# Optimization experiments

Hardware: AMD Instinct MI355X
Metric: run time of the kernel (lower is better)

Reference implementation:

```python
import jax, jax.numpy as jnp
import numpy as np
import math

B, S, D = 1, 4096, 2048
H, KVH, HD = 32, 8, 64
W = 512            # sliding window size (== block size)
THETA = 10000.0
EPS = 1e-5
INTER = 5632
PRE_SCALE = 1.0 / math.sqrt(2.0)


def setup_inputs() -> dict:
    key = jax.random.key(0)
    ks = jax.random.split(key, 8)
    def w(k, shape, fan_in):
        return jax.random.normal(k, shape, jnp.float32) * (fan_in ** -0.5)
    return {
        "hidden_states": jax.random.normal(ks[0], (B, S, D), jnp.float32),
        "mixer_norm_w": jnp.ones((D,), jnp.float32),
        "wq": w(ks[1], (D, H * HD), D),
        "wk": w(ks[2], (D, KVH * HD), D),
        "wv": w(ks[3], (D, KVH * HD), D),
        "wo": w(ks[4], (H * HD, D), H * HD),
        "mlp_norm_w": jnp.ones((D,), jnp.float32),
        "w_gate": w(ks[5], (D, 2 * INTER), D),
        "w_down": w(ks[6], (INTER, D), INTER),
    }


def rmsnorm(x, w, eps=EPS):
    return x * jax.lax.rsqrt(jnp.mean(x * x, axis=-1, keepdims=True) + eps) * w


def rope(x):
    # x: [B, S, h, HD]; rotate-half RoPE
    half = HD // 2
    inv_freq = 1.0 / (THETA ** (jnp.arange(0, HD, 2, dtype=jnp.float32) / HD))
    freqs = jnp.arange(S, dtype=jnp.float32)[:, None] * inv_freq[None, :]  # [S, half]
    cos = jnp.cos(freqs)[None, :, None, :]
    sin = jnp.sin(freqs)[None, :, None, :]
    x1, x2 = x[..., :half], x[..., half:]
    return jnp.concatenate([x1 * cos - x2 * sin, x2 * cos + x1 * sin], axis=-1)


def sliding_attention(x, wq, wk, wv, wo):
    # x already pre-scaled; returns attn output (pre /pre_scale)
    q = (x @ wq).reshape(B, S, H, HD)
    k = (x @ wk).reshape(B, S, KVH, HD)
    v = (x @ wv).reshape(B, S, KVH, HD)
    q, k = rope(q), rope(k)
    rep = H // KVH
    k = jnp.repeat(k, rep, axis=2)  # [B,S,H,HD]
    v = jnp.repeat(v, rep, axis=2)
    nb = S // W
    qb = q.reshape(B, nb, W, H, HD)
    kb = k.reshape(B, nb, W, H, HD)
    vb = v.reshape(B, nb, W, H, HD)
    zeros = jnp.zeros((B, 1, W, H, HD), q.dtype)
    kw = jnp.concatenate([jnp.concatenate([zeros, kb[:, :-1]], axis=1), kb], axis=2)  # [B,nb,2W,H,HD]
    vw = jnp.concatenate([jnp.concatenate([zeros, vb[:, :-1]], axis=1), vb], axis=2)
    # local mask [nb, W, 2W]
    blk = jnp.arange(nb)[:, None, None]
    q_pos = blk * W + jnp.arange(W)[None, :, None]
    k_pos = blk * W - W + jnp.arange(2 * W)[None, None, :]
    mask = (k_pos >= 0) & (k_pos <= q_pos) & (q_pos - k_pos < W)
    scores = jnp.einsum("bnqhd,bnkhd->bhnqk", qb, kw) * (HD ** -0.5)
    scores = jnp.where(mask[None, None], scores, jnp.finfo(scores.dtype).min)
    p = jax.nn.softmax(scores, axis=-1)
    out = jnp.einsum("bhnqk,bnkhd->bnqhd", p, vw).reshape(B, S, H * HD)
    return out @ wo


def reference(hidden_states, mixer_norm_w, wq, wk, wv, wo, mlp_norm_w, w_gate, w_down):
    residual = hidden_states
    x = rmsnorm(hidden_states, mixer_norm_w)
    attn_out = sliding_attention(x * PRE_SCALE, wq, wk, wv, wo) / PRE_SCALE
    h = residual + attn_out
    xn = rmsnorm(h, mlp_norm_w)
    gv = xn @ w_gate
    gate, y = gv[..., :INTER], gv[..., INTER:]
    mlp_out = (jax.nn.silu(gate) * y) @ w_down
    return h + mlp_out
```

## Files before the change

### kernel.cpp

```cpp
#include <hip/hip_runtime.h>
#include <stdint.h>

typedef __attribute__((ext_vector_type(8))) short s16x8;
typedef __attribute__((ext_vector_type(4))) float f32x4;

#define GLD_LDS16(gp, lp) __builtin_amdgcn_global_load_lds( \
    (__attribute__((address_space(1))) void*)(void*)(gp), \
    (__attribute__((address_space(3))) void*)(lp), 16, 0, 0)

__device__ __forceinline__ float b2f(unsigned short s) {
    unsigned int u = ((unsigned int)s) << 16;
    return __builtin_bit_cast(float, u);
}
__device__ __forceinline__ unsigned short f2b(float f) {
    unsigned int u = __builtin_bit_cast(unsigned int, f);
    u = (u + 0x7FFFu + ((u >> 16) & 1u)) >> 16;
    return (unsigned short)u;
}
__device__ __forceinline__ f32x4 mfma16(s16x8 a, s16x8 b, f32x4 c) {
    return __builtin_amdgcn_mfma_f32_16x16x32_bf16(a, b, c, 0, 0, 0);
}

__global__ __launch_bounds__(256) void rmsnorm_bf16(
    const float* __restrict__ x, const float* __restrict__ wgt,
    unsigned short* __restrict__ out)
{
    const int row = blockIdx.x;
    const int t = threadIdx.x;
    const float* xr = x + (size_t)row * 2048;
    float4 a = *(const float4*)(xr + t * 8);
    float4 b = *(const float4*)(xr + t * 8 + 4);
    float ss = a.x*a.x + a.y*a.y + a.z*a.z + a.w*a.w
             + b.x*b.x + b.y*b.y + b.z*b.z + b.w*b.w;
    #pragma unroll
    for (int d = 1; d < 64; d <<= 1) ss += __shfl_xor(ss, d);
    __shared__ float red[4];
    if ((t & 63) == 0) red[t >> 6] = ss;
    __syncthreads();
    float tot = red[0] + red[1] + red[2] + red[3];
    float inv = rsqrtf(tot * (1.0f / 2048.0f) + 1e-5f);
    float vals[8] = {a.x, a.y, a.z, a.w, b.x, b.y, b.z, b.w};
    const float* wr_ = wgt + t * 8;
    s16x8 ov;
    #pragma unroll
    for (int j = 0; j < 8; ++j) ov[j] = (short)f2b(vals[j] * inv * wr_[j]);
    *(s16x8*)(out + (size_t)row * 2048 + t * 8) = ov;
}

__global__ __launch_bounds__(256) void transpose_to_bf16(
    const float* __restrict__ in, unsigned short* __restrict__ out, int K, int N)
{
    __shared__ float tile[64][65];
    const int n0 = blockIdx.x * 64, k0 = blockIdx.y * 64;
    const int t = threadIdx.x;
    const int kr = t >> 4, nc = (t & 15) * 4;
    #pragma unroll
    for (int i = 0; i < 4; ++i) {
        float4 v = *(const float4*)(in + (size_t)(k0 + kr + i * 16) * N + n0 + nc);
        tile[nc + 0][kr + i * 16] = v.x;
        tile[nc + 1][kr + i * 16] = v.y;
        tile[nc + 2][kr + i * 16] = v.z;
        tile[nc + 3][kr + i * 16] = v.w;
    }
    __syncthreads();
    const int nr = t >> 3, kc = (t & 7) * 8;
    #pragma unroll
    for (int p = 0; p < 2; ++p) {
        s16x8 o;
        #pragma unroll
        for (int j = 0; j < 8; ++j) o[j] = (short)f2b(tile[nr + p * 32][kc + j]);
        *(s16x8*)(out + (size_t)(n0 + nr + p * 32) * K + k0 + kc) = o;
    }
}

template <int BN, int EPI>
__global__ __launch_bounds__(512, 2) void gemmq(
    const unsigned short* __restrict__ A,
    const unsigned short* __restrict__ B,
    void* __restrict__ Cv,
    const float* __restrict__ ADD,
    const float2* __restrict__ RT,
    int N, int K)
{
    constexpr int WN  = BN / 4;
    constexpr int HN  = WN / 2;
    constexpr int NJQ = WN / 32;
    constexpr int NBU = BN / 64;
    constexpr int ABUF = 256 * 64;
    constexpr int BBUF = BN * 64;
    __shared__ __align__(16) unsigned short As[2 * ABUF];
    __shared__ __align__(16) unsigned short Bs[2 * BBUF];

    const int t = threadIdx.x;
    const int l = t & 63, w = t >> 6;
    const int l15 = l & 15, lg = l >> 4;
    const int wr = w >> 2, wc = w & 3;
    const int x7 = l15 & 7;
    const int cc0 = ((lg) ^ x7) << 3;
    const int cc1 = ((4 | lg) ^ x7) << 3;

    const int nwg = (int)gridDim.x;
    const int orig = (int)blockIdx.x;
    const int q8 = nwg >> 3, r8 = nwg & 7;
    const int xcd = orig & 7, lid = orig >> 3;
    const int wg = (xcd < r8 ? xcd * (q8 + 1) : r8 * (q8 + 1) + (xcd - r8) * q8) + lid;
    const int m0 = (wg & 15) * 256;
    const int n0 = (wg >> 4) * BN;

    const int tr = t >> 3;
    const int scol = ((t & 7) ^ (tr & 7)) << 3;
    const unsigned short* pA[4];
    #pragma unroll
    for (int u = 0; u < 4; ++u) {
        const int lrow = u * 64 + tr;
        const int g = ((lrow >> 6) & 1) * 128 + (lrow >> 7) * 64 + (lrow & 63);
        pA[u] = A + (size_t)(m0 + g) * K + scol;
    }
    const unsigned short* pB[NBU];
    #pragma unroll
    for (int u = 0; u < NBU; ++u) {
        const int lrow = u * 64 + tr;
        const int h = lrow / (BN / 2), rem = lrow % (BN / 2);
        const int g = (rem / HN) * WN + h * HN + (rem % HN);
        pB[u] = B + (size_t)(n0 + g) * K + scol;
    }

    f32x4 acc[2][2][4][NJQ] = {};
    s16x8 aF[4][2];
    s16x8 bF[2][NJQ][2];

    const int NT = K / 64;

    #pragma unroll
    for (int u = 0; u < 4; ++u) GLD_LDS16(pA[u], &As[u * 4096 + t * 8]);
    #pragma unroll
    for (int u = 0; u < NBU; ++u) GLD_LDS16(pB[u], &Bs[u * 4096 + t * 8]);
    asm volatile("s_waitcnt vmcnt(0)" ::: "memory");
    __builtin_amdgcn_s_barrier();

    for (int kt = 0; kt < NT; ++kt) {
        const int rb  = (kt & 1) ? ABUF : 0;
        const int rbB = (kt & 1) ? BBUF : 0;
        const int wb  = ABUF - rb;
        const int wbB = BBUF - rbB;
        const int knext = (kt + 1 < NT ? kt + 1 : kt) * 64;

        #pragma unroll
        for (int i = 0; i < 4; ++i) {
            const int lr = wr * 64 + i * 16 + l15;
            aF[i][0] = *(const s16x8*)&As[rb + lr * 64 + cc0];
            aF[i][1] = *(const s16x8*)&As[rb + lr * 64 + cc1];
        }
        #pragma unroll
        for (int j = 0; j < NJQ; ++j) {
            const int lr = wc * HN + j * 16 + l15;
            bF[0][j][0] = *(const s16x8*)&Bs[rbB + lr * 64 + cc0];
            bF[0][j][1] = *(const s16x8*)&Bs[rbB + lr * 64 + cc1];
        }
        #pragma unroll
        for (int u = 0; u < 4; ++u)
            GLD_LDS16(pA[u] + knext, &As[wb + u * 4096 + t * 8]);
        #pragma unroll
        for (int kk = 0; kk < 2; ++kk)
            #pragma unroll
            for (int i = 0; i < 4; ++i)
                #pragma unroll
                for (int j = 0; j < NJQ; ++j)
                    acc[0][0][i][j] = mfma16(aF[i][kk], bF[0][j][kk], acc[0][0][i][j]);

        #pragma unroll
        for (int j = 0; j < NJQ; ++j) {
            const int lr = (BN / 2) + wc * HN + j * 16 + l15;
            bF[1][j][0] = *(const s16x8*)&Bs[rbB + lr * 64 + cc0];
            bF[1][j][1] = *(const s16x8*)&Bs[rbB + lr * 64 + cc1];
        }
        #pragma unroll
        for (int u = 0; u < NBU; ++u)
            GLD_LDS16(pB[u] + knext, &Bs[wbB + u * 4096 + t * 8]);
        #pragma unroll
        for (int kk = 0; kk < 2; ++kk)
            #pragma unroll
            for (int i = 0; i < 4; ++i)
                #pragma unroll
                for (int j = 0; j < NJQ; ++j)
                    acc[0][1][i][j] = mfma16(aF[i][kk], bF[1][j][kk], acc[0][1][i][j]);

        #pragma unroll
        for (int i = 0; i < 4; ++i) {
            const int lr = 128 + wr * 64 + i * 16 + l15;
            aF[i][0] = *(const s16x8*)&As[rb + lr * 64 + cc0];
            aF[i][1] = *(const s16x8*)&As[rb + lr * 64 + cc1];
        }
        #pragma unroll
        for (int kk = 0; kk < 2; ++kk)
            #pragma unroll
            for (int i = 0; i < 4; ++i)
                #pragma unroll
                for (int j = 0; j < NJQ; ++j)
                    acc[1][0][i][j] = mfma16(aF[i][kk], bF[0][j][kk], acc[1][0][i][j]);

        #pragma unroll
        for (int kk = 0; kk < 2; ++kk)
            #pragma unroll
            for (int i = 0; i < 4; ++i)
                #pragma unroll
                for (int j = 0; j < NJQ; ++j)
                    acc[1][1][i][j] = mfma16(aF[i][kk], bF[1][j][kk], acc[1][1][i][j]);

        asm volatile("s_waitcnt vmcnt(0)" ::: "memory");
        __builtin_amdgcn_s_barrier();
    }

    if constexpr (EPI == 2) {
        unsigned short* Cb = (unsigned short*)Cv;
        const bool roped = (n0 < 2560);
        #pragma unroll
        for (int qm = 0; qm < 2; ++qm)
            #pragma unroll
            for (int i = 0; i < 4; ++i)
                #pragma unroll
                for (int r = 0; r < 4; ++r) {
                    const int row = m0 + wr * 128 + qm * 64 + i * 16 + lg * 4 + r;
                    const size_t rbase = (size_t)row * N;
                    #pragma unroll
                    for (int j = 0; j < NJQ; ++j) {
                        const int d = j * 16 + l15;
                        const int c0 = n0 + wc * WN + j * 16 + l15;
                        float a = acc[qm][0][i][j][r];
                        float b = acc[qm][1][i][j][r];
                        if (roped) {
                            float2 cs = RT[row * 32 + d];
                            Cb[rbase + c0]      = f2b(a * cs.x - b * cs.y);
                            Cb[rbase + c0 + HN] = f2b(b * cs.x + a * cs.y);
                        } else {
                            Cb[rbase + c0]      = f2b(a);
                            Cb[rbase + c0 + HN] = f2b(b);
                        }
                    }
                }
    } else {
        #pragma unroll
        for (int qm = 0; qm < 2; ++qm)
            #pragma unroll
            for (int i = 0; i < 4; ++i)
                #pragma unroll
                for (int r = 0; r < 4; ++r) {
                    const int row = m0 + wr * 128 + qm * 64 + i * 16 + lg * 4 + r;
                    const size_t rbase = (size_t)row * N;
                    #pragma unroll
                    for (int qn = 0; qn < 2; ++qn)
                        #pragma unroll
                        for (int j = 0; j < NJQ; ++j) {
                            const int col = n0 + wc * WN + qn * HN + j * 16 + l15;
                            float v = acc[qm][qn][i][j][r];
                            if constexpr (EPI == 0) {
                                ((unsigned short*)Cv)[rbase + col] = f2b(v);
                            } else {
                                ((float*)Cv)[rbase + col] = v + ADD[rbase + col];
                            }
                        }
                }
    }
}

__global__ __launch_bounds__(512, 2) void gemm_glu(
    const unsigned short* __restrict__ A,
    const unsigned short* __restrict__ Bg,
    const unsigned short* __restrict__ By,
    unsigned short* __restrict__ act,
    int N, int K)
{
    constexpr int ABUF = 256 * 64, BBUF = 128 * 64;
    __shared__ __align__(16) unsigned short As[2 * ABUF];
    __shared__ __align__(16) unsigned short Bgs[2 * BBUF];
    __shared__ __align__(16) unsigned short Bys[2 * BBUF];

    const int t = threadIdx.x;
    const int l = t & 63, w = t >> 6;
    const int l15 = l & 15, lg = l >> 4;
    const int wr = w >> 2, wc = w & 3;
    const int x7 = l15 & 7;
    const int cc0 = ((lg) ^ x7) << 3;
    const int cc1 = ((4 | lg) ^ x7) << 3;

    const int nwg = (int)gridDim.x;
    const int orig = (int)blockIdx.x;
    const int q8 = nwg >> 3;
    const int xcd = orig & 7, lid = orig >> 3;
    const int wg = xcd * q8 + lid;
    const int m0 = (wg & 15) * 256;
    const int n0 = (wg >> 4) * 128;

    const int tr = t >> 3;
    const int scol = ((t & 7) ^ (tr & 7)) << 3;
    const unsigned short* pA[4];
    #pragma unroll
    for (int u = 0; u < 4; ++u) {
        const int lrow = u * 64 + tr;
        const int g = ((lrow >> 6) & 1) * 128 + (lrow >> 7) * 64 + (lrow & 63);
        pA[u] = A + (size_t)(m0 + g) * K + scol;
    }
    const unsigned short *pG[2], *pY[2];
    #pragma unroll
    for (int u = 0; u < 2; ++u) {
        const int g = (tr >> 4) * 32 + u * 16 + (tr & 15);
        pG[u] = Bg + (size_t)(n0 + g) * K + scol;
        pY[u] = By + (size_t)(n0 + g) * K + scol;
    }

    f32x4 accG[2][2][4] = {};
    f32x4 accY[2][2][4] = {};
    s16x8 aF[4][2];
    s16x8 gF[2][2], yF[2][2];

    const int NT = K / 64;

    #pragma unroll
    for (int u = 0; u < 4; ++u) GLD_LDS16(pA[u], &As[u * 4096 + t * 8]);
    GLD_LDS16(pG[0], &Bgs[0 * 4096 + t * 8]);
    GLD_LDS16(pY[0], &Bys[0 * 4096 + t * 8]);
    GLD_LDS16(pG[1], &Bgs[1 * 4096 + t * 8]);
    GLD_LDS16(pY[1], &Bys[1 * 4096 + t * 8]);
    asm volatile("s_waitcnt vmcnt(0)" ::: "memory");
    __builtin_amdgcn_s_barrier();

    for (int kt = 0; kt < NT; ++kt) {
        const int rb  = (kt & 1) ? ABUF : 0;
        const int rbB = (kt & 1) ? BBUF : 0;
        const int wb  = ABUF - rb;
        const int wbB = BBUF - rbB;
        const int knext = (kt + 1 < NT ? kt + 1 : kt) * 64;

        #pragma unroll
        for (int i = 0; i < 4; ++i) {
            const int lr = wr * 64 + i * 16 + l15;
            aF[i][0] = *(const s16x8*)&As[rb + lr * 64 + cc0];
            aF[i][1] = *(const s16x8*)&As[rb + lr * 64 + cc1];
        }
        {
            const int lr = wc * 16 + l15;
            gF[0][0] = *(const s16x8*)&Bgs[rbB + lr * 64 + cc0];
            gF[0][1] = *(const s16x8*)&Bgs[rbB + lr * 64 + cc1];
            yF[0][0] = *(const s16x8*)&Bys[rbB + lr * 64 + cc0];
            yF[0][1] = *(const s16x8*)&Bys[rbB + lr * 64 + cc1];
        }
        #pragma unroll
        for (int u = 0; u < 4; ++u)
            GLD_LDS16(pA[u] + knext, &As[wb + u * 4096 + t * 8]);
        #pragma unroll
        for (int kk = 0; kk < 2; ++kk)
            #pragma unroll
            for (int i = 0; i < 4; ++i) {
                accG[0][0][i] = mfma16(aF[i][kk], gF[0][kk], accG[0][0][i]);
                accY[0][0][i] = mfma16(aF[i][kk], yF[0][kk], accY[0][0][i]);
            }

        {
            const int lr = 64 + wc * 16 + l15;
            gF[1][0] = *(const s16x8*)&Bgs[rbB + lr * 64 + cc0];
            gF[1][1] = *(const s16x8*)&Bgs[rbB + lr * 64 + cc1];
            yF[1][0] = *(const s16x8*)&Bys[rbB + lr * 64 + cc0];
            yF[1][1] = *(const s16x8*)&Bys[rbB + lr * 64 + cc1];
        }
        GLD_LDS16(pG[0] + knext, &Bgs[wbB + 0 * 4096 + t * 8]);
        GLD_LDS16(pY[0] + knext, &Bys[wbB + 0 * 4096 + t * 8]);
        GLD_LDS16(pG[1] + knext, &Bgs[wbB + 1 * 4096 + t * 8]);
        GLD_LDS16(pY[1] + knext, &Bys[wbB + 1 * 4096 + t * 8]);
        #pragma unroll
        for (int kk = 0; kk < 2; ++kk)
            #pragma unroll
            for (int i = 0; i < 4; ++i) {
                accG[0][1][i] = mfma16(aF[i][kk], gF[1][kk], accG[0][1][i]);
                accY[0][1][i] = mfma16(aF[i][kk], yF[1][kk], accY[0][1][i]);
            }

        #pragma unroll
        for (int i = 0; i < 4; ++i) {
            const int lr = 128 + wr * 64 + i * 16 + l15;
            aF[i][0] = *(const s16x8*)&As[rb + lr * 64 + cc0];
            aF[i][1] = *(const s16x8*)&As[rb + lr * 64 + cc1];
        }
        #pragma unroll
        for (int kk = 0; kk < 2; ++kk)
            #pragma unroll
            for (int i = 0; i < 4; ++i) {
                accG[1][0][i] = mfma16(aF[i][kk], gF[0][kk], accG[1][0][i]);
                accY[1][0][i] = mfma16(aF[i][kk], yF[0][kk], accY[1][0][i]);
            }

        #pragma unroll
        for (int kk = 0; kk < 2; ++kk)
            #pragma unroll
            for (int i = 0; i < 4; ++i) {
                accG[1][1][i] = mfma16(aF[i][kk], gF[1][kk], accG[1][1][i]);
                accY[1][1][i] = mfma16(aF[i][kk], yF[1][kk], accY[1][1][i]);
            }

        asm volatile("s_waitcnt vmcnt(0)" ::: "memory");
        __builtin_amdgcn_s_barrier();
    }

    #pragma unroll
    for (int qm = 0; qm < 2; ++qm)
        #pragma unroll
        for (int i = 0; i < 4; ++i)
            #pragma unroll
            for (int r = 0; r < 4; ++r) {
                const int row = m0 + wr * 128 + qm * 64 + i * 16 + lg * 4 + r;
                const size_t rbase = (size_t)row * N;
                #pragma unroll
                for (int qn = 0; qn < 2; ++qn) {
                    const int col = n0 + wc * 32 + qn * 16 + l15;
                    float g = accG[qm][qn][i][r];
                    float y = accY[qm][qn][i][r];
                    float sg = g / (1.0f + expf(-g));
                    act[rbase + col] = f2b(sg * y);
                }
            }
}

__global__ void rope_tab_k(float2* __restrict__ tab) {
    int i = blockIdx.x * 256 + threadIdx.x;
    if (i >= 4096 * 32) return;
    int s = i >> 5, d = i & 31;
    float inv = exp2f(-(float)d * (13.287712379549449f / 32.0f));
    float fr = (float)s * inv;
    float sv, cv;
    sincosf(fr, &sv, &cv);
    tab[i] = make_float2(cv, sv);
}

__global__ __launch_bounds__(256) void attn_swa(
    const unsigned short* __restrict__ qkv,
    unsigned short* __restrict__ out)
{
    constexpr int LDQ = 3072;
    const int qb = blockIdx.x;
    const int h = blockIdx.y;
    const int kvh = h >> 2;
    const int q0 = qb * 64;
    const int t = threadIdx.x, l = t & 63, w = t >> 6;
    const int l15 = l & 15, lg = l >> 4;

    __shared__ unsigned short Kl[2][64 * 64];
    __shared__ unsigned short Vt[2][64 * 72];
    __shared__ unsigned short Pl[4 * 16 * 72];

    s16x8 qf[2];
    {
        const unsigned short* qp = qkv + (size_t)(q0 + w * 16 + l15) * LDQ + h * 64 + lg * 8;
        qf[0] = *(const s16x8*)(qp);
        qf[1] = *(const s16x8*)(qp + 32);
    }
    float m_run[4] = {-1e30f, -1e30f, -1e30f, -1e30f};
    float l_run[4] = {0.f, 0.f, 0.f, 0.f};
    f32x4 o[4] = {};

    const float SC = 0.0625f * 1.4426950408889634f;
    const int kt_lo = qb >= 8 ? qb - 8 : 0;

    {
        const int ks = kt_lo * 64;
        const unsigned short* kg = qkv + (size_t)(ks + (t >> 3)) * LDQ + 2048 + kvh * 64 + (t & 7) * 8;
        GLD_LDS16(kg, &Kl[0][t * 8]);
        GLD_LDS16(kg + (size_t)32 * LDQ, &Kl[0][t * 8 + 2048]);
        const unsigned short* vg = qkv + (size_t)(ks + l) * LDQ + 2560 + kvh * 64 + w * 16;
        s16x8 v0 = *(const s16x8*)vg;
        s16x8 v1 = *(const s16x8*)(vg + 8);
        #pragma unroll
        for (int j = 0; j < 8; ++j) Vt[0][(w * 16 + j) * 72 + l] = (unsigned short)v0[j];
        #pragma unroll
        for (int j = 0; j < 8; ++j) Vt[0][(w * 16 + 8 + j) * 72 + l] = (unsigned short)v1[j];
        asm volatile("s_waitcnt vmcnt(0)" ::: "memory");
        __syncthreads();
    }

    for (int kt = kt_lo; kt <= qb; ++kt) {
        const int ks = kt * 64;
        const int cur = (kt - kt_lo) & 1;
        const int nxt = cur ^ 1;
        const bool pre = (kt < qb);

        s16x8 v0n, v1n;
        if (pre) {
            const int ks1 = ks + 64;
            const unsigned short* kg = qkv + (size_t)(ks1 + (t >> 3)) * LDQ + 2048 + kvh * 64 + (t & 7) * 8;
            GLD_LDS16(kg, &Kl[nxt][t * 8]);
            GLD_LDS16(kg + (size_t)32 * LDQ, &Kl[nxt][t * 8 + 2048]);
            const unsigned short* vg = qkv + (size_t)(ks1 + l) * LDQ + 2560 + kvh * 64 + w * 16;
            v0n = *(const s16x8*)vg;
            v1n = *(const s16x8*)(vg + 8);
        }

        f32x4 sf[4] = {};
        #pragma unroll
        for (int kf = 0; kf < 4; ++kf) {
            #pragma unroll
            for (int kk = 0; kk < 2; ++kk) {
                s16x8 kb = *(const s16x8*)(&Kl[cur][(kf * 16 + l15) * 64 + kk * 32 + lg * 8]);
                sf[kf] = mfma16(qf[kk], kb, sf[kf]);
            }
        }

        float tmax[4];
        #pragma unroll
        for (int r = 0; r < 4; ++r) {
            int qrow = q0 + w * 16 + lg * 4 + r;
            float mx = -1e30f;
            #pragma unroll
            for (int kf = 0; kf < 4; ++kf) {
                int key = ks + kf * 16 + l15;
                bool valid = (key <= qrow) && (qrow - key < 512);
                if (valid) mx = fmaxf(mx, sf[kf][r]);
            }
            #pragma unroll
            for (int d2 = 1; d2 < 16; d2 <<= 1) mx = fmaxf(mx, __shfl_xor(mx, d2));
            tmax[r] = mx;
        }

        float alpha[4], rsum[4];
        #pragma unroll
        for (int r = 0; r < 4; ++r) {
            float mnew = fmaxf(m_run[r], tmax[r]);
            alpha[r] = exp2f((m_run[r] - mnew) * SC);
            m_run[r] = mnew;
            rsum[r] = 0.f;
        }

        unsigned short* Pw = Pl + w * (16 * 72);
        #pragma unroll
        for (int kf = 0; kf < 4; ++kf) {
            #pragma unroll
            for (int r = 0; r < 4; ++r) {
                int qrow = q0 + w * 16 + lg * 4 + r;
                int key = ks + kf * 16 + l15;
                bool valid = (key <= qrow) && (qrow - key < 512);
                float p = valid ? exp2f((sf[kf][r] - m_run[r]) * SC) : 0.f;
                rsum[r] += p;
                Pw[(lg * 4 + r) * 72 + kf * 16 + l15] = f2b(p);
            }
        }
        #pragma unroll
        for (int r = 0; r < 4; ++r) {
            #pragma unroll
            for (int d2 = 1; d2 < 16; d2 <<= 1) rsum[r] += __shfl_xor(rsum[r], d2);
            l_run[r] = l_run[r] * alpha[r] + rsum[r];
        }
        #pragma unroll
        for (int hf = 0; hf < 4; ++hf)
            #pragma unroll
            for (int r = 0; r < 4; ++r) o[hf][r] *= alpha[r];

        if (pre) {
            #pragma unroll
            for (int j = 0; j < 8; ++j) Vt[nxt][(w * 16 + j) * 72 + l] = (unsigned short)v0n[j];
            #pragma unroll
            for (int j = 0; j < 8; ++j) Vt[nxt][(w * 16 + 8 + j) * 72 + l] = (unsigned short)v1n[j];
        }

        asm volatile("s_waitcnt lgkmcnt(0)" ::: "memory");
        __builtin_amdgcn_sched_barrier(0);

        #pragma unroll
        for (int kk2 = 0; kk2 < 2; ++kk2) {
            s16x8 pa = *(const s16x8*)(Pw + l15 * 72 + kk2 * 32 + lg * 8);
            #pragma unroll
            for (int hf = 0; hf < 4; ++hf) {
                s16x8 vb = *(const s16x8*)(&Vt[cur][(hf * 16 + l15) * 72 + kk2 * 32 + lg * 8]);
                o[hf] = mfma16(pa, vb, o[hf]);
            }
        }

        asm volatile("s_waitcnt vmcnt(0)" ::: "memory");
        __syncthreads();
    }

    #pragma unroll
    for (int r = 0; r < 4; ++r) {
        int qrow = q0 + w * 16 + lg * 4 + r;
        float invl = 1.0f / l_run[r];
        unsigned short* orow = out + (size_t)qrow * 2048 + h * 64;
        #pragma unroll
        for (int hf = 0; hf < 4; ++hf)
            orow[hf * 16 + l15] = f2b(o[hf][r] * invl);
    }
}

extern "C" void kernel_launch(void* const* d_in, const int* in_sizes, int n_in,
                              void* d_out, int out_size, void* d_ws, size_t ws_size,
                              hipStream_t stream)
{
    const float* hidden = (const float*)d_in[0];
    const float* w_mix  = (const float*)d_in[1];
    const float* wq     = (const float*)d_in[2];
    const float* wk     = (const float*)d_in[3];
    const float* wv     = (const float*)d_in[4];
    const float* wo     = (const float*)d_in[5];
    const float* w_mlp  = (const float*)d_in[6];
    const float* wg     = (const float*)d_in[7];
    const float* wd     = (const float*)d_in[8];
    float* out = (float*)d_out;

    char* ws = (char*)d_ws;
    size_t off = 0;
    auto alloc = [&](size_t bytes) {
        char* p = ws + off;
        off += (bytes + 255) & ~(size_t)255;
        return p;
    };
    unsigned short* Wt   = (unsigned short*)alloc((size_t)11264 * 2048 * 2);
    unsigned short* xn   = (unsigned short*)alloc((size_t)4096 * 2048 * 2);
    unsigned short* qkv  = (unsigned short*)alloc((size_t)4096 * 3072 * 2);
    float2*         rtab = (float2*)alloc((size_t)4096 * 32 * 8);
    unsigned short* attn = (unsigned short*)alloc((size_t)4096 * 2048 * 2);
    float*          hbuf = (float*)alloc((size_t)4096 * 2048 * 4);
    unsigned short* act  = (unsigned short*)alloc((size_t)4096 * 5632 * 2);

    rope_tab_k<<<(4096 * 32 + 255) / 256, 256, 0, stream>>>(rtab);

    rmsnorm_bf16<<<4096, 256, 0, stream>>>(hidden, w_mix, xn);

    transpose_to_bf16<<<dim3(32, 32), 256, 0, stream>>>(wq, Wt, 2048, 2048);
    transpose_to_bf16<<<dim3(8, 32), 256, 0, stream>>>(wk, Wt + (size_t)2048 * 2048, 2048, 512);
    transpose_to_bf16<<<dim3(8, 32), 256, 0, stream>>>(wv, Wt + (size_t)2560 * 2048, 2048, 512);

    gemmq<256, 2><<<192, 512, 0, stream>>>(xn, Wt, qkv, nullptr, rtab, 3072, 2048);

    attn_swa<<<dim3(64, 32), 256, 0, stream>>>(qkv, attn);

    transpose_to_bf16<<<dim3(32, 32), 256, 0, stream>>>(wo, Wt, 2048, 2048);
    gemmq<128, 1><<<256, 512, 0, stream>>>(attn, Wt, hbuf, hidden, nullptr, 2048, 2048);

    rmsnorm_bf16<<<4096, 256, 0, stream>>>(hbuf, w_mlp, xn);

    transpose_to_bf16<<<dim3(176, 32), 256, 0, stream>>>(wg, Wt, 2048, 11264);
    gemm_glu<<<704, 512, 0, stream>>>(xn, Wt, Wt + (size_t)5632 * 2048, act, 5632, 2048);

    transpose_to_bf16<<<dim3(32, 88), 256, 0, stream>>>(wd, Wt, 5632, 2048);
    gemmq<128, 1><<<256, 512, 0, stream>>>(act, Wt, out, hbuf, nullptr, 2048, 5632);
}
```

Baseline: 584.2 us.

## Raise wave priority around GEMM MFMA blocks and single-buffer attention K/V tiles

Wraps each MFMA cluster in both GEMM kernels with s_setprio(1)/s_setprio(0), so waves issuing matrix work get scheduler priority over waves issuing loads. Separately, the attention kernel's double-buffered K/V LDS prefetch is replaced by a single buffer that is loaded synchronously at the top of each key tile, with two barriers per tile. This halves attention LDS use, which could allow more resident blocks, but removes the overlap of global loads with compute in that kernel.

```diff
diff --git a/kernel.cpp b/kernel.cpp
--- a/kernel.cpp
+++ b/kernel.cpp
@@ -160,6 +160,7 @@
         #pragma unroll
         for (int u = 0; u < 4; ++u)
             GLD_LDS16(pA[u] + knext, &As[wb + u * 4096 + t * 8]);
+        __builtin_amdgcn_s_setprio(1);
         #pragma unroll
         for (int kk = 0; kk < 2; ++kk)
             #pragma unroll
@@ -167,6 +168,7 @@
                 #pragma unroll
                 for (int j = 0; j < NJQ; ++j)
                     acc[0][0][i][j] = mfma16(aF[i][kk], bF[0][j][kk], acc[0][0][i][j]);
+        __builtin_amdgcn_s_setprio(0);
 
         #pragma unroll
         for (int j = 0; j < NJQ; ++j) {
@@ -177,6 +179,7 @@
         #pragma unroll
         for (int u = 0; u < NBU; ++u)
             GLD_LDS16(pB[u] + knext, &Bs[wbB + u * 4096 + t * 8]);
+        __builtin_amdgcn_s_setprio(1);
         #pragma unroll
         for (int kk = 0; kk < 2; ++kk)
             #pragma unroll
@@ -184,6 +187,7 @@
                 #pragma unroll
                 for (int j = 0; j < NJQ; ++j)
                     acc[0][1][i][j] = mfma16(aF[i][kk], bF[1][j][kk], acc[0][1][i][j]);
+        __builtin_amdgcn_s_setprio(0);
 
         #pragma unroll
         for (int i = 0; i < 4; ++i) {
@@ -191,6 +195,7 @@
             aF[i][0] = *(const s16x8*)&As[rb + lr * 64 + cc0];
             aF[i][1] = *(const s16x8*)&As[rb + lr * 64 + cc1];
         }
+        __builtin_amdgcn_s_setprio(1);
         #pragma unroll
         for (int kk = 0; kk < 2; ++kk)
             #pragma unroll
@@ -198,7 +203,9 @@
                 #pragma unroll
                 for (int j = 0; j < NJQ; ++j)
                     acc[1][0][i][j] = mfma16(aF[i][kk], bF[0][j][kk], acc[1][0][i][j]);
-
+        __builtin_amdgcn_s_setprio(0);
+
+        __builtin_amdgcn_s_setprio(1);
         #pragma unroll
         for (int kk = 0; kk < 2; ++kk)
             #pragma unroll
@@ -206,6 +213,7 @@
                 #pragma unroll
                 for (int j = 0; j < NJQ; ++j)
                     acc[1][1][i][j] = mfma16(aF[i][kk], bF[1][j][kk], acc[1][1][i][j]);
+        __builtin_amdgcn_s_setprio(0);
 
         asm volatile("s_waitcnt vmcnt(0)" ::: "memory");
         __builtin_amdgcn_s_barrier();
@@ -347,6 +355,7 @@
         #pragma unroll
         for (int u = 0; u < 4; ++u)
             GLD_LDS16(pA[u] + knext, &As[wb + u * 4096 + t * 8]);
+        __builtin_amdgcn_s_setprio(1);
         #pragma unroll
         for (int kk = 0; kk < 2; ++kk)
             #pragma unroll
@@ -354,6 +363,7 @@
                 accG[0][0][i] = mfma16(aF[i][kk], gF[0][kk], accG[0][0][i]);
                 accY[0][0][i] = mfma16(aF[i][kk], yF[0][kk], accY[0][0][i]);
             }
+        __builtin_amdgcn_s_setprio(0);
 
         {
             const int lr = 64 + wc * 16 + l15;
@@ -366,6 +376,7 @@
         GLD_LDS16(pY[0] + knext, &Bys[wbB + 0 * 4096 + t * 8]);
         GLD_LDS16(pG[1] + knext, &Bgs[wbB + 1 * 4096 + t * 8]);
         GLD_LDS16(pY[1] + knext, &Bys[wbB + 1 * 4096 + t * 8]);
+        __builtin_amdgcn_s_setprio(1);
         #pragma unroll
         for (int kk = 0; kk < 2; ++kk)
             #pragma unroll
@@ -373,6 +384,7 @@
                 accG[0][1][i] = mfma16(aF[i][kk], gF[1][kk], accG[0][1][i]);
                 accY[0][1][i] = mfma16(aF[i][kk], yF[1][kk], accY[0][1][i]);
             }
+        __builtin_amdgcn_s_setprio(0);
 
         #pragma unroll
         for (int i = 0; i < 4; ++i) {
@@ -380,6 +392,7 @@
             aF[i][0] = *(const s16x8*)&As[rb + lr * 64 + cc0];
             aF[i][1] = *(const s16x8*)&As[rb + lr * 64 + cc1];
         }
+        __builtin_amdgcn_s_setprio(1);
         #pragma unroll
         for (int kk = 0; kk < 2; ++kk)
             #pragma unroll
@@ -387,7 +400,9 @@
                 accG[1][0][i] = mfma16(aF[i][kk], gF[0][kk], accG[1][0][i]);
                 accY[1][0][i] = mfma16(aF[i][kk], yF[0][kk], accY[1][0][i]);
             }
-
+        __builtin_amdgcn_s_setprio(0);
+
+        __builtin_amdgcn_s_setprio(1);
         #pragma unroll
         for (int kk = 0; kk < 2; ++kk)
             #pragma unroll
@@ -395,6 +410,7 @@
                 accG[1][1][i] = mfma16(aF[i][kk], gF[1][kk], accG[1][1][i]);
                 accY[1][1][i] = mfma16(aF[i][kk], yF[1][kk], accY[1][1][i]);
             }
+        __builtin_amdgcn_s_setprio(0);
 
         asm volatile("s_waitcnt vmcnt(0)" ::: "memory");
         __builtin_amdgcn_s_barrier();
@@ -442,8 +458,8 @@
     const int t = threadIdx.x, l = t & 63, w = t >> 6;
     const int l15 = l & 15, lg = l >> 4;
 
-    __shared__ unsigned short Kl[2][64 * 64];
-    __shared__ unsigned short Vt[2][64 * 72];
+    __shared__ unsigned short Kl[64 * 64];
+    __shared__ unsigned short Vt[64 * 72];
     __shared__ unsigned short Pl[4 * 16 * 72];
 
     s16x8 qf[2];
@@ -459,45 +475,31 @@
     const float SC = 0.0625f * 1.4426950408889634f;
     const int kt_lo = qb >= 8 ? qb - 8 : 0;
 
-    {
-        const int ks = kt_lo * 64;
-        const unsigned short* kg = qkv + (size_t)(ks + (t >> 3)) * LDQ + 2048 + kvh * 64 + (t & 7) * 8;
-        GLD_LDS16(kg, &Kl[0][t * 8]);
-        GLD_LDS16(kg + (size_t)32 * LDQ, &Kl[0][t * 8 + 2048]);
-        const unsigned short* vg = qkv + (size_t)(ks + l) * LDQ + 2560 + kvh * 64 + w * 16;
-        s16x8 v0 = *(const s16x8*)vg;
-        s16x8 v1 = *(const s16x8*)(vg + 8);
-        #pragma unroll
-        for (int j = 0; j < 8; ++j) Vt[0][(w * 16 + j) * 72 + l] = (unsigned short)v0[j];
-        #pragma unroll
-        for (int j = 0; j < 8; ++j) Vt[0][(w * 16 + 8 + j) * 72 + l] = (unsigned short)v1[j];
-        asm volatile("s_waitcnt vmcnt(0)" ::: "memory");
-        __syncthreads();
-    }
-
     for (int kt = kt_lo; kt <= qb; ++kt) {
         const int ks = kt * 64;
-        const int cur = (kt - kt_lo) & 1;
-        const int nxt = cur ^ 1;
-        const bool pre = (kt < qb);
-
-        s16x8 v0n, v1n;
-        if (pre) {
-            const int ks1 = ks + 64;
-            const unsigned short* kg = qkv + (size_t)(ks1 + (t >> 3)) * LDQ + 2048 + kvh * 64 + (t & 7) * 8;
-            GLD_LDS16(kg, &Kl[nxt][t * 8]);
-            GLD_LDS16(kg + (size_t)32 * LDQ, &Kl[nxt][t * 8 + 2048]);
-            const unsigned short* vg = qkv + (size_t)(ks1 + l) * LDQ + 2560 + kvh * 64 + w * 16;
-            v0n = *(const s16x8*)vg;
-            v1n = *(const s16x8*)(vg + 8);
-        }
+        __syncthreads();
+        {
+            const unsigned short* kg = qkv + (size_t)(ks + (t >> 3)) * LDQ + 2048 + kvh * 64 + (t & 7) * 8;
+            GLD_LDS16(kg, Kl + t * 8);
+            GLD_LDS16(kg + (size_t)32 * LDQ, Kl + t * 8 + 2048);
+        }
+        {
+            const unsigned short* vg = qkv + (size_t)(ks + l) * LDQ + 2560 + kvh * 64 + w * 16;
+            s16x8 v0 = *(const s16x8*)vg;
+            s16x8 v1 = *(const s16x8*)(vg + 8);
+            #pragma unroll
+            for (int j = 0; j < 8; ++j) Vt[(w * 16 + j) * 72 + l] = (unsigned short)v0[j];
+            #pragma unroll
+            for (int j = 0; j < 8; ++j) Vt[(w * 16 + 8 + j) * 72 + l] = (unsigned short)v1[j];
+        }
+        __syncthreads();
 
         f32x4 sf[4] = {};
         #pragma unroll
         for (int kf = 0; kf < 4; ++kf) {
             #pragma unroll
             for (int kk = 0; kk < 2; ++kk) {
-                s16x8 kb = *(const s16x8*)(&Kl[cur][(kf * 16 + l15) * 64 + kk * 32 + lg * 8]);
+                s16x8 kb = *(const s16x8*)(Kl + (kf * 16 + l15) * 64 + kk * 32 + lg * 8);
                 sf[kf] = mfma16(qf[kk], kb, sf[kf]);
             }
         }
@@ -551,13 +553,6 @@
             #pragma unroll
             for (int r = 0; r < 4; ++r) o[hf][r] *= alpha[r];
 
-        if (pre) {
-            #pragma unroll
-            for (int j = 0; j < 8; ++j) Vt[nxt][(w * 16 + j) * 72 + l] = (unsigned short)v0n[j];
-            #pragma unroll
-            for (int j = 0; j < 8; ++j) Vt[nxt][(w * 16 + 8 + j) * 72 + l] = (unsigned short)v1n[j];
-        }
-
         asm volatile("s_waitcnt lgkmcnt(0)" ::: "memory");
         __builtin_amdgcn_sched_barrier(0);
 
@@ -566,13 +561,10 @@
             s16x8 pa = *(const s16x8*)(Pw + l15 * 72 + kk2 * 32 + lg * 8);
             #pragma unroll
             for (int hf = 0; hf < 4; ++hf) {
-                s16x8 vb = *(const s16x8*)(&Vt[cur][(hf * 16 + l15) * 72 + kk2 * 32 + lg * 8]);
+                s16x8 vb = *(const s16x8*)(Vt + (hf * 16 + l15) * 72 + kk2 * 32 + lg * 8);
                 o[hf] = mfma16(pa, vb, o[hf]);
             }
         }
-
-        asm volatile("s_waitcnt vmcnt(0)" ::: "memory");
-        __syncthreads();
     }
 
     #pragma unroll
```

Result: faster. 544.1 us (-6.9%).
